# Kernel tuning notes

Hardware: AMD Instinct MI355X
Metric: run time of the kernel (lower is better)

## Reference

```python
import jax, jax.numpy as jnp
import numpy as np

LAYERS = 5      # lstm_layers
H = 1           # lstm_hidden_size
IN = 21         # 9 (rot) + 6 (v) + 6 (u)
NEG = 0.1       # LeakyReLU negative slope
EPS = 1e-5      # BatchNorm1d eps


def _lstm_cell(x, h, c, w_ih, w_hh):
    # torch gate order: i, f, g, o ; no biases (lstm_bias=False)
    gates = x @ w_ih.T + h @ w_hh.T              # [k, 4H]
    i, f, g, o = jnp.split(gates, 4, axis=-1)
    i = jax.nn.sigmoid(i)
    f = jax.nn.sigmoid(f)
    g = jnp.tanh(g)
    o = jax.nn.sigmoid(o)
    c_new = f * c + i * g
    h_new = o * jnp.tanh(c_new)
    return h_new, c_new


def _bn_train(z, gamma, beta):
    # BatchNorm1d in training mode: batch stats, biased variance
    m = z.mean(axis=0)
    var = z.var(axis=0)
    return gamma * (z - m) / jnp.sqrt(var + EPS) + beta


def setup_inputs() -> dict:
    key = jax.random.key(0)
    ks = jax.random.split(key, 14)
    k, T = 65536, 32
    s = 0.2  # init scale, roughly torch uniform(-1/sqrt(H)) magnitude
    inp = {
        "r": jax.random.normal(ks[0], (k, T, 9), jnp.float32),
        "v": jax.random.normal(ks[1], (k, T, 6), jnp.float32),
        "u": jax.random.normal(ks[2], (k, T, 6), jnp.float32),
        # LSTM weights: layer 0 sees IN features, layers 1..4 see H
        "w_ih0": jax.random.normal(ks[3], (4 * H, IN), jnp.float32) * s,
        "w_ih_rest": jax.random.normal(ks[4], (LAYERS - 1, 4 * H, H), jnp.float32) * s,
        "w_hh": jax.random.normal(ks[5], (LAYERS, 4 * H, H), jnp.float32) * s,
        # FC head: Linear(H,32,no bias) -> BN -> LReLU -> Linear(32,32) -> BN -> LReLU -> Linear(32,6)
        "W1": jax.random.normal(ks[6], (32, H), jnp.float32) * s,
        "g1": jnp.ones((32,), jnp.float32),
        "b1": jnp.zeros((32,), jnp.float32),
        "W2": jax.random.normal(ks[7], (32, 32), jnp.float32) * s,
        "g2": jnp.ones((32,), jnp.float32),
        "b2": jnp.zeros((32,), jnp.float32),
        "W3": jax.random.normal(ks[8], (6, 32), jnp.float32) * s,
    }
    return inp


def reference(r, v, u, w_ih0, w_ih_rest, w_hh, W1, g1, b1, W2, g2, b2, W3):
    x = jnp.concatenate([r, v, u], axis=-1)          # [k, T, 21]
    k = x.shape[0]
    h0 = jnp.zeros((LAYERS, k, H), x.dtype)
    c0 = jnp.zeros((LAYERS, k, H), x.dtype)
    xs = jnp.swapaxes(x, 0, 1)                       # [T, k, 21]

    def step(carry, xt):
        h, c = carry
        hs, cs = [], []
        layer_in = xt
        for l in range(LAYERS):
            w_ih = w_ih0 if l == 0 else w_ih_rest[l - 1]
            hl, cl = _lstm_cell(layer_in, h[l], c[l], w_ih, w_hh[l])
            hs.append(hl)
            cs.append(cl)
            layer_in = hl
        return (jnp.stack(hs), jnp.stack(cs)), layer_in  # top-layer output

    (hT, cT), outs = jax.lax.scan(step, (h0, c0), xs)    # outs: [T, k, H]

    # fc applied to out[:, 0] -> first timestep of top layer
    y = outs[0]                                          # [k, H]
    y = jax.nn.leaky_relu(_bn_train(y @ W1.T, g1, b1), NEG)
    y = jax.nn.leaky_relu(_bn_train(y @ W2.T, g2, b2), NEG)
    dv = y @ W3.T                                        # [k, 6]
    return dv[:, None], hT, cT
```

## Files before the change

### kernel.cpp

```cpp
#include <hip/hip_runtime.h>
#include <math.h>

#define T 32
#define NEGS 0.1f
#define EPS 1e-5f
#define NREG 33


__device__ __forceinline__ float rcp_fast(float x) { return __builtin_amdgcn_rcpf(x); }
__device__ __forceinline__ float sigm(float x) { return rcp_fast(1.0f + __expf(-x)); }
__device__ __forceinline__ float tanh_fast(float x) {
    float t = __expf(2.0f * fabsf(x));
    float r = 1.0f - 2.0f * rcp_fast(t + 1.0f);
    return copysignf(r, x);
}
__device__ __forceinline__ float lrelu(float x) { return x > 0.0f ? x : NEGS * x; }

__device__ __forceinline__ void bn1_params(const float* __restrict__ W1,
                                           const float* __restrict__ g1,
                                           const float* __restrict__ b1,
                                           const double* __restrict__ wsd, int k, int j,
                                           float& my, float& vy, float& a, float& b,
                                           float& tau, int& flip)
{
    my = (float)(wsd[0] / k);
    vy = (float)(wsd[1] / k) - my * my;
    float wj = W1[j];
    a = g1[j] * wj * rsqrtf(fmaf(wj * wj, vy, EPS));
    b = b1[j];
    if (a > 0.0f)      { tau = my - b / a; flip = 0; }
    else if (a < 0.0f) { tau = my - b / a; flip = 1; }
    else               { tau = (b > 0.0f ? -__builtin_inff() : __builtin_inff()); flip = 0; }
}

__global__ __launch_bounds__(256, 1)
void fused_kernel(const float* __restrict__ r, const float* __restrict__ v,
                  const float* __restrict__ u, const float* __restrict__ wih0,
                  const float* __restrict__ wihr, const float* __restrict__ whhp,
                  float* __restrict__ out, double* __restrict__ wsd,
                  float* __restrict__ wsy, int k)
{
    __shared__ float rbuf[8 * 32 * 9];
    __shared__ float vbuf[8 * 32 * 6];
    __shared__ float ubuf[8 * 32 * 6];
    __shared__ float4 pbuf[32][9];
    const int tid = threadIdx.x;
    const int sBase = blockIdx.x * 256;

    float4* rb4 = reinterpret_cast<float4*>(rbuf);
    float4* vb4 = reinterpret_cast<float4*>(vbuf);
    float4* ub4 = reinterpret_cast<float4*>(ubuf);

    float wi0[4][21];
#pragma unroll
    for (int g = 0; g < 4; ++g)
#pragma unroll
        for (int j = 0; j < 21; ++j) wi0[g][j] = wih0[g * 21 + j];
    float wir[4][4];
#pragma unroll
    for (int l = 0; l < 4; ++l)
#pragma unroll
        for (int g = 0; g < 4; ++g) wir[l][g] = wihr[l * 4 + g];
    float whh[5][4];
#pragma unroll
    for (int l = 0; l < 5; ++l)
#pragma unroll
        for (int g = 0; g < 4; ++g) whh[l][g] = whhp[l * 4 + g];

    float4 gbuf[T];

    float4 Ra0, Ra1, Ra2, Rv0, Rv1, Ru0, Ru1;

#define ISSUE_GROUP(gg)                                                         \
    do {                                                                        \
        const int s0_ = sBase + (gg) * 8;                                       \
        const float4* r4_ = reinterpret_cast<const float4*>(r + (size_t)s0_ * (T * 9)); \
        const float4* v4_ = reinterpret_cast<const float4*>(v + (size_t)s0_ * (T * 6)); \
        const float4* u4_ = reinterpret_cast<const float4*>(u + (size_t)s0_ * (T * 6)); \
        Ra0 = r4_[tid];                                                         \
        Ra1 = r4_[256 + tid];                                                   \
        if (tid < 64) Ra2 = r4_[512 + tid];                                     \
        Rv0 = v4_[tid];                                                         \
        if (tid < 128) Rv1 = v4_[256 + tid];                                    \
        Ru0 = u4_[tid];                                                         \
        if (tid < 128) Ru1 = u4_[256 + tid];                                    \
    } while (0)

    ISSUE_GROUP(0);

    for (int sg = 0; sg < 32; ++sg) {
        rb4[tid] = Ra0;
        rb4[256 + tid] = Ra1;
        if (tid < 64) rb4[512 + tid] = Ra2;
        vb4[tid] = Rv0;
        if (tid < 128) vb4[256 + tid] = Rv1;
        ub4[tid] = Ru0;
        if (tid < 128) ub4[256 + tid] = Ru1;

        if (sg < 31) ISSUE_GROUP(sg + 1);

        __syncthreads();

        const int sl = tid >> 5, t = tid & 31;
        float x[21];
#pragma unroll
        for (int j = 0; j < 9; ++j) x[j] = rbuf[sl * (32 * 9) + t * 9 + j];
#pragma unroll
        for (int j = 0; j < 6; ++j) x[9 + j] = vbuf[sl * (32 * 6) + t * 6 + j];
#pragma unroll
        for (int j = 0; j < 6; ++j) x[15 + j] = ubuf[sl * (32 * 6) + t * 6 + j];

        float4 g4;
        float* gp = (float*)&g4;
#pragma unroll
        for (int gi = 0; gi < 4; ++gi) {
            float acc = 0.f;
#pragma unroll
            for (int j = 0; j < 21; ++j) acc = fmaf(wi0[gi][j], x[j], acc);
            gp[gi] = acc;
        }
        pbuf[t][sl] = g4;
        __syncthreads();

        if ((tid >> 3) == sg) {
            const int l = tid & 7;
#pragma unroll
            for (int tt = 0; tt < T; ++tt) gbuf[tt] = pbuf[tt][l];
        }
    }
#undef ISSUE_GROUP

    const int s = sBase + tid;
    float h[5] = {0.f, 0.f, 0.f, 0.f, 0.f};
    float c[5] = {0.f, 0.f, 0.f, 0.f, 0.f};
    float y0 = 0.f;

#pragma unroll
    for (int t = 0; t < T; ++t) {
        const float4 G = gbuf[t];
        float a0 = fmaf(whh[0][0], h[0], G.x);
        float a1 = fmaf(whh[0][1], h[0], G.y);
        float a2 = fmaf(whh[0][2], h[0], G.z);
        float a3 = fmaf(whh[0][3], h[0], G.w);
        {
            float ii = sigm(a0), ff = sigm(a1);
            float gg = tanh_fast(a2), oo = sigm(a3);
            c[0] = ff * c[0] + ii * gg;
            h[0] = oo * tanh_fast(c[0]);
        }
        float xin = h[0];
#pragma unroll
        for (int l = 1; l < 5; ++l) {
            float b0 = fmaf(wir[l - 1][0], xin, whh[l][0] * h[l]);
            float b1 = fmaf(wir[l - 1][1], xin, whh[l][1] * h[l]);
            float b2 = fmaf(wir[l - 1][2], xin, whh[l][2] * h[l]);
            float b3 = fmaf(wir[l - 1][3], xin, whh[l][3] * h[l]);
            float ii = sigm(b0), ff = sigm(b1);
            float gg = tanh_fast(b2), oo = sigm(b3);
            c[l] = ff * c[l] + ii * gg;
            h[l] = oo * tanh_fast(c[l]);
            xin = h[l];
        }
        if (t == 0) y0 = h[4];
    }

#pragma unroll
    for (int l = 0; l < 5; ++l) {
        out[(size_t)6 * k + (size_t)l * k + s] = h[l];
        out[(size_t)11 * k + (size_t)l * k + s] = c[l];
    }
    wsy[s] = y0;

    float ys = y0, yq = y0 * y0;
#pragma unroll
    for (int off = 32; off; off >>= 1) {
        ys += __shfl_down(ys, off);
        yq += __shfl_down(yq, off);
    }
    __shared__ float pS[4], pQ[4];
    const int wid = threadIdx.x >> 6, lane = threadIdx.x & 63;
    if (lane == 0) { pS[wid] = ys; pQ[wid] = yq; }
    __syncthreads();
    if (threadIdx.x == 0) {
        atomicAdd(&wsd[0], (double)(pS[0] + pS[1] + pS[2] + pS[3]));
        atomicAdd(&wsd[1], (double)(pQ[0] + pQ[1] + pQ[2] + pQ[3]));
    }
}

__global__ __launch_bounds__(256)
void hist_kernel(const float* __restrict__ W1, const float* __restrict__ g1,
                 const float* __restrict__ b1, double* __restrict__ wsd,
                 const float* __restrict__ wsy, int k)
{
    __shared__ float sTau[32];
    __shared__ float sH[3 * NREG];
    __shared__ float sMy;
    const int tid = threadIdx.x;
    if (tid < 3 * NREG) sH[tid] = 0.f;
    if (tid < 32) {
        float my, vy, a, b, tau; int flip;
        bn1_params(W1, g1, b1, wsd, k, tid, my, vy, a, b, tau, flip);
        sTau[tid] = tau;
        if (tid == 0) sMy = my;
    }
    __syncthreads();
    const int stride = gridDim.x * 256;
    for (int s = blockIdx.x * 256 + tid; s < k; s += stride) {
        const float y = wsy[s];
        const float yc = y - sMy;
        int rgn = 0;
#pragma unroll
        for (int j = 0; j < 32; ++j) rgn += (y > sTau[j]) ? 1 : 0;
        atomicAdd(&sH[rgn], 1.0f);
        atomicAdd(&sH[NREG + rgn], yc);
        atomicAdd(&sH[2 * NREG + rgn], yc * yc);
    }
    __syncthreads();
    if (tid < 3 * NREG) atomicAdd(&wsd[2 + tid], (double)sH[tid]);
}

__global__ __launch_bounds__(256)
void tables_kernel(const float* __restrict__ W1, const float* __restrict__ g1,
                   const float* __restrict__ b1, const float* __restrict__ W2,
                   const float* __restrict__ g2, const float* __restrict__ b2,
                   const double* __restrict__ wsd, float* __restrict__ gPQ, int k)
{
    __shared__ float sA[32], sB[32], sTau[32];
    __shared__ int sRank[32], sFlip[32];
    __shared__ float sS0[NREG], sS1[NREG], sS2[NREG];
    __shared__ float sW2[1024];
    __shared__ float sSumY1[32];
    __shared__ float sM[1024];
    __shared__ float sI2[32], sM2v[32], sB2[32];
    const int tid = threadIdx.x;

    for (int i = tid; i < 1024; i += 256) sW2[i] = W2[i];
    if (tid < NREG) {
        sS0[tid] = (float)wsd[2 + tid];
        sS1[tid] = (float)wsd[2 + NREG + tid];
        sS2[tid] = (float)wsd[2 + 2 * NREG + tid];
    }
    if (tid < 32) {
        float my, vy, a, b, tau; int flip;
        bn1_params(W1, g1, b1, wsd, k, tid, my, vy, a, b, tau, flip);
        sA[tid] = a; sB[tid] = b; sTau[tid] = tau; sFlip[tid] = flip;
        sB2[tid] = b2[tid];
    }
    __syncthreads();
    if (tid < 32) {
        int rk = 0;
        float tj = sTau[tid];
#pragma unroll
        for (int l = 0; l < 32; ++l)
            rk += (sTau[l] < tj || (sTau[l] == tj && l < tid)) ? 1 : 0;
        sRank[tid] = rk;
    }
    __syncthreads();
    if (tid < 32) {
        const int rk = sRank[tid], fl = sFlip[tid];
        const float a = sA[tid], b = sB[tid];
        float acc = 0.f;
        for (int rg = 0; rg < NREG; ++rg) {
            float m = (((rk < rg) ? 1 : 0) != fl) ? 1.0f : NEGS;
            acc += m * (a * sS1[rg] + b * sS0[rg]);
        }
        sSumY1[tid] = acc;
    }
    for (int p = tid; p < 1024; p += 256) {
        const int j = p >> 5, l = p & 31;
        const int rj = sRank[j], fj = sFlip[j];
        const int rl = sRank[l], flp = sFlip[l];
        const float aj = sA[j], bj = sB[j], al = sA[l], bl = sB[l];
        const float caa = aj * al, cab = aj * bl + al * bj, cbb = bj * bl;
        float acc = 0.f;
        for (int rg = 0; rg < NREG; ++rg) {
            float mj = (((rj < rg) ? 1 : 0) != fj) ? 1.0f : NEGS;
            float ml = (((rl < rg) ? 1 : 0) != flp) ? 1.0f : NEGS;
            acc += mj * ml * (caa * sS2[rg] + cab * sS1[rg] + cbb * sS0[rg]);
        }
        sM[p] = acc;
    }
    __syncthreads();
    if (tid < 32) {
        const int i = tid;
        float s2 = 0.f, ss2 = 0.f;
#pragma unroll
        for (int j = 0; j < 32; ++j) {
            float wij = sW2[i * 32 + j];
            s2 = fmaf(wij, sSumY1[j], s2);
            float tj = 0.f;
#pragma unroll
            for (int l = 0; l < 32; ++l) tj = fmaf(sW2[i * 32 + l], sM[j * 32 + l], tj);
            ss2 = fmaf(wij, tj, ss2);
        }
        float m2 = s2 / k;
        float v2 = ss2 / k - m2 * m2;
        sM2v[i] = m2;
        sI2[i] = g2[i] * rsqrtf(v2 + EPS);
    }
    __syncthreads();
    for (int idx = tid; idx < NREG * 32; idx += 256) {
        const int rg = idx >> 5, i = idx & 31;
        float Ai = 0.f, Bi = 0.f;
#pragma unroll
        for (int j = 0; j < 32; ++j) {
            float m = (((sRank[j] < rg) ? 1 : 0) != sFlip[j]) ? 1.0f : NEGS;
            float w = sW2[i * 32 + j] * m;
            Ai = fmaf(w, sA[j], Ai);
            Bi = fmaf(w, sB[j], Bi);
        }
        gPQ[idx] = sI2[i] * Ai;
        gPQ[NREG * 32 + idx] = sI2[i] * (Bi - sM2v[i]) + sB2[i];
    }
}

__global__ __launch_bounds__(256)
void final_kernel(const float* __restrict__ W1, const float* __restrict__ g1,
                  const float* __restrict__ b1, const float* __restrict__ W3,
                  const double* __restrict__ wsd, const float* __restrict__ wsy,
                  const float* __restrict__ gPQ, float* __restrict__ out, int k)
{
    __shared__ float sTau[32], sW3[192], sMy;
    __shared__ float sP[NREG][33], sQ[NREG][33];
    const int tid = threadIdx.x;
    for (int idx = tid; idx < NREG * 32; idx += 256) {
        const int rg = idx >> 5, i = idx & 31;
        sP[rg][i] = gPQ[idx];
        sQ[rg][i] = gPQ[NREG * 32 + idx];
    }
    if (tid < 192) sW3[tid] = W3[tid];
    if (tid < 32) {
        float my, vy, a, b, tau; int flip;
        bn1_params(W1, g1, b1, wsd, k, tid, my, vy, a, b, tau, flip);
        sTau[tid] = tau;
        if (tid == 0) sMy = my;
    }
    __syncthreads();
    const int s = blockIdx.x * 256 + tid;
    const float y = wsy[s];
    const float yc = y - sMy;
    int rgn = 0;
#pragma unroll
    for (int j = 0; j < 32; ++j) rgn += (y > sTau[j]) ? 1 : 0;
    float dv[6] = {0.f, 0.f, 0.f, 0.f, 0.f, 0.f};
#pragma unroll
    for (int i = 0; i < 32; ++i) {
        float y2 = lrelu(fmaf(sP[rgn][i], yc, sQ[rgn][i]));
#pragma unroll
        for (int m = 0; m < 6; ++m) dv[m] = fmaf(sW3[m * 32 + i], y2, dv[m]);
    }
#pragma unroll
    for (int m = 0; m < 6; ++m) out[(size_t)s * 6 + m] = dv[m];
}

extern "C" void kernel_launch(void* const* d_in, const int* in_sizes, int n_in,
                              void* d_out, int out_size, void* d_ws, size_t ws_size,
                              hipStream_t stream)
{
    const float* r    = (const float*)d_in[0];
    const float* v    = (const float*)d_in[1];
    const float* u    = (const float*)d_in[2];
    const float* wih0 = (const float*)d_in[3];
    const float* wihr = (const float*)d_in[4];
    const float* whhp = (const float*)d_in[5];
    const float* W1   = (const float*)d_in[6];
    const float* g1v  = (const float*)d_in[7];
    const float* b1v  = (const float*)d_in[8];
    const float* W2   = (const float*)d_in[9];
    const float* g2v  = (const float*)d_in[10];
    const float* b2v  = (const float*)d_in[11];
    const float* W3   = (const float*)d_in[12];

    const int k = in_sizes[0] / (T * 9);
    float* out = (float*)d_out;
    double* wsd = (double*)d_ws;
    float* wsy = (float*)((char*)d_ws + 1024);
    float* gPQ = (float*)((char*)d_ws + 1024 + (size_t)k * 4);

    hipMemsetAsync(d_ws, 0, 1024, stream);

    const int blocks = k / 256;
    fused_kernel<<<blocks, 256, 0, stream>>>(r, v, u, wih0, wihr, whhp,
                                             out, wsd, wsy, k);
    hist_kernel<<<64, 256, 0, stream>>>(W1, g1v, b1v, wsd, wsy, k);
    tables_kernel<<<1, 256, 0, stream>>>(W1, g1v, b1v, W2, g2v, b2v, wsd, gPQ, k);
    final_kernel<<<blocks, 256, 0, stream>>>(W1, g1v, b1v, W3, wsd, wsy, gPQ, out, k);
}
```

Measured before the change: 262.7 us.

## Double-buffer shared staging and prefetch two groups ahead in input projection loop

The input-projection phase now uses two shared-memory buffers for the raw inputs and the partial gate results. It keeps two register sets of prefetched global loads, issued two groups ahead. The gather of gate results into each thread's register buffer is delayed by one iteration, which removes one __syncthreads per group and deepens load latency hiding. The cost is double the LDS footprint and roughly 28 more live VGPRs on top of an already large per-thread register array, which risks spills.

Measured after the change: 258.5 us (median of 2 runs). Within noise of the previous version (-1.6%).

```diff
diff --git a/kernel.cpp b/kernel.cpp
--- a/kernel.cpp
+++ b/kernel.cpp
@@ -40,17 +40,13 @@
                   float* __restrict__ out, double* __restrict__ wsd,
                   float* __restrict__ wsy, int k)
 {
-    __shared__ float rbuf[8 * 32 * 9];
-    __shared__ float vbuf[8 * 32 * 6];
-    __shared__ float ubuf[8 * 32 * 6];
-    __shared__ float4 pbuf[32][9];
+    __shared__ float rbuf[2][8 * 32 * 9];
+    __shared__ float vbuf[2][8 * 32 * 6];
+    __shared__ float ubuf[2][8 * 32 * 6];
+    __shared__ float4 pbuf[2][32][9];
     const int tid = threadIdx.x;
     const int sBase = blockIdx.x * 256;
 
-    float4* rb4 = reinterpret_cast<float4*>(rbuf);
-    float4* vb4 = reinterpret_cast<float4*>(vbuf);
-    float4* ub4 = reinterpret_cast<float4*>(ubuf);
-
     float wi0[4][21];
 #pragma unroll
     for (int g = 0; g < 4; ++g)
@@ -69,66 +65,78 @@
 
     float4 gbuf[T];
 
-    float4 Ra0, Ra1, Ra2, Rv0, Rv1, Ru0, Ru1;
-
-#define ISSUE_GROUP(gg)                                                         \
+    float4 Aa0, Aa1, Aa2, Av0, Av1, Au0, Au1;
+    float4 Ba0, Ba1, Ba2, Bv0, Bv1, Bu0, Bu1;
+
+#define ISSUE(gg, R0, R1, R2, V0, V1, U0, U1)                                   \
     do {                                                                        \
         const int s0_ = sBase + (gg) * 8;                                       \
         const float4* r4_ = reinterpret_cast<const float4*>(r + (size_t)s0_ * (T * 9)); \
         const float4* v4_ = reinterpret_cast<const float4*>(v + (size_t)s0_ * (T * 6)); \
         const float4* u4_ = reinterpret_cast<const float4*>(u + (size_t)s0_ * (T * 6)); \
-        Ra0 = r4_[tid];                                                         \
-        Ra1 = r4_[256 + tid];                                                   \
-        if (tid < 64) Ra2 = r4_[512 + tid];                                     \
-        Rv0 = v4_[tid];                                                         \
-        if (tid < 128) Rv1 = v4_[256 + tid];                                    \
-        Ru0 = u4_[tid];                                                         \
-        if (tid < 128) Ru1 = u4_[256 + tid];                                    \
+        R0 = r4_[tid];                                                          \
+        R1 = r4_[256 + tid];                                                    \
+        if (tid < 64) R2 = r4_[512 + tid];                                      \
+        V0 = v4_[tid];                                                          \
+        if (tid < 128) V1 = v4_[256 + tid];                                     \
+        U0 = u4_[tid];                                                          \
+        if (tid < 128) U1 = u4_[256 + tid];                                     \
     } while (0)
 
-    ISSUE_GROUP(0);
-
-    for (int sg = 0; sg < 32; ++sg) {
-        rb4[tid] = Ra0;
-        rb4[256 + tid] = Ra1;
-        if (tid < 64) rb4[512 + tid] = Ra2;
-        vb4[tid] = Rv0;
-        if (tid < 128) vb4[256 + tid] = Rv1;
-        ub4[tid] = Ru0;
-        if (tid < 128) ub4[256 + tid] = Ru1;
-
-        if (sg < 31) ISSUE_GROUP(sg + 1);
-
-        __syncthreads();
-
-        const int sl = tid >> 5, t = tid & 31;
-        float x[21];
-#pragma unroll
-        for (int j = 0; j < 9; ++j) x[j] = rbuf[sl * (32 * 9) + t * 9 + j];
-#pragma unroll
-        for (int j = 0; j < 6; ++j) x[9 + j] = vbuf[sl * (32 * 6) + t * 6 + j];
-#pragma unroll
-        for (int j = 0; j < 6; ++j) x[15 + j] = ubuf[sl * (32 * 6) + t * 6 + j];
-
-        float4 g4;
-        float* gp = (float*)&g4;
-#pragma unroll
-        for (int gi = 0; gi < 4; ++gi) {
-            float acc = 0.f;
-#pragma unroll
-            for (int j = 0; j < 21; ++j) acc = fmaf(wi0[gi][j], x[j], acc);
-            gp[gi] = acc;
-        }
-        pbuf[t][sl] = g4;
-        __syncthreads();
-
-        if ((tid >> 3) == sg) {
-            const int l = tid & 7;
-#pragma unroll
-            for (int tt = 0; tt < T; ++tt) gbuf[tt] = pbuf[tt][l];
-        }
-    }
-#undef ISSUE_GROUP
+#define BODY(sg, p, R0, R1, R2, V0, V1, U0, U1)                                 \
+    do {                                                                        \
+        float4* rb4_ = reinterpret_cast<float4*>(rbuf[p]);                      \
+        float4* vb4_ = reinterpret_cast<float4*>(vbuf[p]);                      \
+        float4* ub4_ = reinterpret_cast<float4*>(ubuf[p]);                      \
+        rb4_[tid] = R0;                                                         \
+        rb4_[256 + tid] = R1;                                                   \
+        if (tid < 64) rb4_[512 + tid] = R2;                                     \
+        vb4_[tid] = V0;                                                         \
+        if (tid < 128) vb4_[256 + tid] = V1;                                    \
+        ub4_[tid] = U0;                                                         \
+        if (tid < 128) ub4_[256 + tid] = U1;                                    \
+        if ((sg) + 2 < 32) ISSUE((sg) + 2, R0, R1, R2, V0, V1, U0, U1);         \
+        __syncthreads();                                                        \
+        if ((sg) > 0 && (tid >> 3) == (sg) - 1) {                               \
+            const int l_ = tid & 7;                                             \
+            _Pragma("unroll")                                                   \
+            for (int tt = 0; tt < T; ++tt) gbuf[tt] = pbuf[1 - (p)][tt][l_];    \
+        }                                                                       \
+        const int sl_ = tid >> 5, t_ = tid & 31;                                \
+        float x_[21];                                                           \
+        _Pragma("unroll")                                                       \
+        for (int j = 0; j < 9; ++j) x_[j] = rbuf[p][sl_ * (32 * 9) + t_ * 9 + j]; \
+        _Pragma("unroll")                                                       \
+        for (int j = 0; j < 6; ++j) x_[9 + j] = vbuf[p][sl_ * (32 * 6) + t_ * 6 + j]; \
+        _Pragma("unroll")                                                       \
+        for (int j = 0; j < 6; ++j) x_[15 + j] = ubuf[p][sl_ * (32 * 6) + t_ * 6 + j]; \
+        float4 g4_;                                                             \
+        float* gp_ = (float*)&g4_;                                              \
+        _Pragma("unroll")                                                       \
+        for (int gi = 0; gi < 4; ++gi) {                                        \
+            float acc_ = 0.f;                                                   \
+            _Pragma("unroll")                                                   \
+            for (int j = 0; j < 21; ++j) acc_ = fmaf(wi0[gi][j], x_[j], acc_);  \
+            gp_[gi] = acc_;                                                     \
+        }                                                                       \
+        pbuf[p][t_][sl_] = g4_;                                                 \
+    } while (0)
+
+    ISSUE(0, Aa0, Aa1, Aa2, Av0, Av1, Au0, Au1);
+    ISSUE(1, Ba0, Ba1, Ba2, Bv0, Bv1, Bu0, Bu1);
+
+    for (int sg2 = 0; sg2 < 32; sg2 += 2) {
+        BODY(sg2,     0, Aa0, Aa1, Aa2, Av0, Av1, Au0, Au1);
+        BODY(sg2 + 1, 1, Ba0, Ba1, Ba2, Bv0, Bv1, Bu0, Bu1);
+    }
+    __syncthreads();
+    if ((tid >> 3) == 31) {
+        const int l_ = tid & 7;
+#pragma unroll
+        for (int tt = 0; tt < T; ++tt) gbuf[tt] = pbuf[1][tt][l_];
+    }
+#undef BODY
+#undef ISSUE
 
     const int s = sBase + tid;
     float h[5] = {0.f, 0.f, 0.f, 0.f, 0.f};
```

## Shrink fused LSTM kernel to single-wave blocks with wave-local LDS fencing

Applied to the files above, without the earlier changes.

The fused LSTM kernel now runs as 64-thread, single-wavefront blocks instead of 256-thread blocks. Each wave stages its own 8-sample groups through LDS. Block-wide __syncthreads are replaced with s_waitcnt lgkmcnt(0) fences, and the cross-wave reduction is replaced by a per-wave atomic. The aim is to remove block barrier stalls and get 4x more blocks for scheduling. The trade-offs are more LDS per resident wave, which caps occupancy, more register pressure from 21 prefetched float4s, and 4x more double atomics.

Measured after the change: 386.0 us. 1.47x slower.

```diff
diff --git a/kernel.cpp b/kernel.cpp
--- a/kernel.cpp
+++ b/kernel.cpp
@@ -15,6 +15,10 @@
     return copysignf(r, x);
 }
 __device__ __forceinline__ float lrelu(float x) { return x > 0.0f ? x : NEGS * x; }
+
+__device__ __forceinline__ void wave_fence() {
+    asm volatile("s_waitcnt lgkmcnt(0)" ::: "memory");
+}
 
 __device__ __forceinline__ void bn1_params(const float* __restrict__ W1,
                                            const float* __restrict__ g1,
@@ -33,23 +37,23 @@
     else               { tau = (b > 0.0f ? -__builtin_inff() : __builtin_inff()); flip = 0; }
 }
 
-__global__ __launch_bounds__(256, 1)
+__global__ __launch_bounds__(64, 1)
 void fused_kernel(const float* __restrict__ r, const float* __restrict__ v,
                   const float* __restrict__ u, const float* __restrict__ wih0,
                   const float* __restrict__ wihr, const float* __restrict__ whhp,
                   float* __restrict__ out, double* __restrict__ wsd,
                   float* __restrict__ wsy, int k)
 {
-    __shared__ float rbuf[8 * 32 * 9];
-    __shared__ float vbuf[8 * 32 * 6];
-    __shared__ float ubuf[8 * 32 * 6];
+    __shared__ float rs[8 * 32 * 9];
+    __shared__ float vs[8 * 32 * 6];
+    __shared__ float us[8 * 32 * 6];
     __shared__ float4 pbuf[32][9];
-    const int tid = threadIdx.x;
-    const int sBase = blockIdx.x * 256;
-
-    float4* rb4 = reinterpret_cast<float4*>(rbuf);
-    float4* vb4 = reinterpret_cast<float4*>(vbuf);
-    float4* ub4 = reinterpret_cast<float4*>(ubuf);
+    const int lane = threadIdx.x;
+    const int wBase = blockIdx.x * 64;
+
+    float4* rs4 = reinterpret_cast<float4*>(rs);
+    float4* vs4 = reinterpret_cast<float4*>(vs);
+    float4* us4 = reinterpret_cast<float4*>(us);
 
     float wi0[4][21];
 #pragma unroll
@@ -69,68 +73,73 @@
 
     float4 gbuf[T];
 
-    float4 Ra0, Ra1, Ra2, Rv0, Rv1, Ru0, Ru1;
-
-#define ISSUE_GROUP(gg)                                                         \
+    float4 P[21];
+
+#define ISSUE(gg)                                                               \
     do {                                                                        \
-        const int s0_ = sBase + (gg) * 8;                                       \
-        const float4* r4_ = reinterpret_cast<const float4*>(r + (size_t)s0_ * (T * 9)); \
-        const float4* v4_ = reinterpret_cast<const float4*>(v + (size_t)s0_ * (T * 6)); \
-        const float4* u4_ = reinterpret_cast<const float4*>(u + (size_t)s0_ * (T * 6)); \
-        Ra0 = r4_[tid];                                                         \
-        Ra1 = r4_[256 + tid];                                                   \
-        if (tid < 64) Ra2 = r4_[512 + tid];                                     \
-        Rv0 = v4_[tid];                                                         \
-        if (tid < 128) Rv1 = v4_[256 + tid];                                    \
-        Ru0 = u4_[tid];                                                         \
-        if (tid < 128) Ru1 = u4_[256 + tid];                                    \
+        const int s0_ = wBase + (gg) * 8;                                       \
+        const float4* r4_ = reinterpret_cast<const float4*>(r + (size_t)s0_ * 288); \
+        const float4* v4_ = reinterpret_cast<const float4*>(v + (size_t)s0_ * 192); \
+        const float4* u4_ = reinterpret_cast<const float4*>(u + (size_t)s0_ * 192); \
+        _Pragma("unroll")                                                       \
+        for (int q = 0; q < 9; ++q) P[q] = r4_[q * 64 + lane];                  \
+        _Pragma("unroll")                                                       \
+        for (int q = 0; q < 6; ++q) P[9 + q] = v4_[q * 64 + lane];              \
+        _Pragma("unroll")                                                       \
+        for (int q = 0; q < 6; ++q) P[15 + q] = u4_[q * 64 + lane];             \
     } while (0)
 
-    ISSUE_GROUP(0);
-
-    for (int sg = 0; sg < 32; ++sg) {
-        rb4[tid] = Ra0;
-        rb4[256 + tid] = Ra1;
-        if (tid < 64) rb4[512 + tid] = Ra2;
-        vb4[tid] = Rv0;
-        if (tid < 128) vb4[256 + tid] = Rv1;
-        ub4[tid] = Ru0;
-        if (tid < 128) ub4[256 + tid] = Ru1;
-
-        if (sg < 31) ISSUE_GROUP(sg + 1);
-
-        __syncthreads();
-
-        const int sl = tid >> 5, t = tid & 31;
-        float x[21];
-#pragma unroll
-        for (int j = 0; j < 9; ++j) x[j] = rbuf[sl * (32 * 9) + t * 9 + j];
-#pragma unroll
-        for (int j = 0; j < 6; ++j) x[9 + j] = vbuf[sl * (32 * 6) + t * 6 + j];
-#pragma unroll
-        for (int j = 0; j < 6; ++j) x[15 + j] = ubuf[sl * (32 * 6) + t * 6 + j];
-
-        float4 g4;
-        float* gp = (float*)&g4;
-#pragma unroll
-        for (int gi = 0; gi < 4; ++gi) {
-            float acc = 0.f;
-#pragma unroll
-            for (int j = 0; j < 21; ++j) acc = fmaf(wi0[gi][j], x[j], acc);
-            gp[gi] = acc;
-        }
-        pbuf[t][sl] = g4;
-        __syncthreads();
-
-        if ((tid >> 3) == sg) {
-            const int l = tid & 7;
+    ISSUE(0);
+
+#pragma unroll
+    for (int g = 0; g < 8; ++g) {
+#pragma unroll
+        for (int q = 0; q < 9; ++q) rs4[q * 64 + lane] = P[q];
+#pragma unroll
+        for (int q = 0; q < 6; ++q) vs4[q * 64 + lane] = P[9 + q];
+#pragma unroll
+        for (int q = 0; q < 6; ++q) us4[q * 64 + lane] = P[15 + q];
+
+        if (g < 7) ISSUE(g + 1);
+
+        wave_fence();
+
+#pragma unroll
+        for (int q = 0; q < 4; ++q) {
+            const int idx = q * 64 + lane;
+            const int sl = idx >> 5, t = idx & 31;
+            float x[21];
+#pragma unroll
+            for (int j = 0; j < 9; ++j) x[j] = rs[sl * 288 + t * 9 + j];
+#pragma unroll
+            for (int j = 0; j < 6; ++j) x[9 + j] = vs[sl * 192 + t * 6 + j];
+#pragma unroll
+            for (int j = 0; j < 6; ++j) x[15 + j] = us[sl * 192 + t * 6 + j];
+            float4 g4;
+            float* gp = (float*)&g4;
+#pragma unroll
+            for (int gi = 0; gi < 4; ++gi) {
+                float acc = 0.f;
+#pragma unroll
+                for (int j = 0; j < 21; ++j) acc = fmaf(wi0[gi][j], x[j], acc);
+                gp[gi] = acc;
+            }
+            pbuf[t][sl] = g4;
+        }
+
+        wave_fence();
+
+        if ((lane >> 3) == g) {
+            const int l = lane & 7;
 #pragma unroll
             for (int tt = 0; tt < T; ++tt) gbuf[tt] = pbuf[tt][l];
         }
-    }
-#undef ISSUE_GROUP
-
-    const int s = sBase + tid;
+
+        wave_fence();
+    }
+#undef ISSUE
+
+    const int s = wBase + lane;
     float h[5] = {0.f, 0.f, 0.f, 0.f, 0.f};
     float c[5] = {0.f, 0.f, 0.f, 0.f, 0.f};
     float y0 = 0.f;
@@ -177,13 +186,9 @@
         ys += __shfl_down(ys, off);
         yq += __shfl_down(yq, off);
     }
-    __shared__ float pS[4], pQ[4];
-    const int wid = threadIdx.x >> 6, lane = threadIdx.x & 63;
-    if (lane == 0) { pS[wid] = ys; pQ[wid] = yq; }
-    __syncthreads();
-    if (threadIdx.x == 0) {
-        atomicAdd(&wsd[0], (double)(pS[0] + pS[1] + pS[2] + pS[3]));
-        atomicAdd(&wsd[1], (double)(pQ[0] + pQ[1] + pQ[2] + pQ[3]));
+    if (lane == 0) {
+        atomicAdd(&wsd[0], (double)ys);
+        atomicAdd(&wsd[1], (double)yq);
     }
 }
 
@@ -379,10 +384,9 @@
 
     hipMemsetAsync(d_ws, 0, 1024, stream);
 
-    const int blocks = k / 256;
-    fused_kernel<<<blocks, 256, 0, stream>>>(r, v, u, wih0, wihr, whhp,
-                                             out, wsd, wsy, k);
+    fused_kernel<<<k / 64, 64, 0, stream>>>(r, v, u, wih0, wihr, whhp,
+                                            out, wsd, wsy, k);
     hist_kernel<<<64, 256, 0, stream>>>(W1, g1v, b1v, wsd, wsy, k);
     tables_kernel<<<1, 256, 0, stream>>>(W1, g1v, b1v, W2, g2v, b2v, wsd, gPQ, k);
-    final_kernel<<<blocks, 256, 0, stream>>>(W1, g1v, b1v, W3, wsd, wsy, gPQ, out, k);
-}
+    final_kernel<<<k / 256, 256, 0, stream>>>(W1, g1v, b1v, W3, wsd, wsy, gPQ, out, k);
+}
```
